# Kernel tuning notes

Measured on AMD Instinct MI355X. Metric: run time of the kernel, lower is better.

The kernel has to match this reference:

```python
import jax, jax.numpy as jnp
import numpy as np
import math

C = 256
GROUPS = 8
EPS = 1e-5


def setup_inputs() -> dict:
    key = jax.random.key(0)
    ks = jax.random.split(key, 12)
    b, c, h, w = 4, C, 64, 64
    s = 1.0 / math.sqrt(c)
    return {
        "x": jax.random.normal(ks[0], (b, c, h, w), dtype=jnp.float32),
        "gamma": jax.random.normal(ks[1], (c,), dtype=jnp.float32) * 0.1 + 1.0,
        "beta": jax.random.normal(ks[2], (c,), dtype=jnp.float32) * 0.1,
        "wq": jax.random.normal(ks[3], (c, c), dtype=jnp.float32) * s,
        "bq": jnp.zeros((c,), dtype=jnp.float32),
        "wk": jax.random.normal(ks[4], (c, c), dtype=jnp.float32) * s,
        "bk": jnp.zeros((c,), dtype=jnp.float32),
        "wv": jax.random.normal(ks[5], (c, c), dtype=jnp.float32) * s,
        "bv": jnp.zeros((c,), dtype=jnp.float32),
        "wp": jax.random.normal(ks[6], (c, c), dtype=jnp.float32) * s,
        "bp": jnp.zeros((c,), dtype=jnp.float32),
    }


def _group_norm(x, gamma, beta):
    b, c, h, w = x.shape
    xg = x.reshape(b, GROUPS, c // GROUPS, h * w)
    mean = xg.mean(axis=(2, 3), keepdims=True)
    var = xg.var(axis=(2, 3), keepdims=True)
    xn = ((xg - mean) * jax.lax.rsqrt(var + EPS)).reshape(b, c, h, w)
    return xn * gamma[None, :, None, None] + beta[None, :, None, None]


def _conv1x1(x, w, b):
    # 1x1 conv == per-pixel channel GEMM
    return jnp.einsum('oc,bchw->bohw', w, x) + b[None, :, None, None]


def reference(x, gamma, beta, wq, bq, wk, bk, wv, bv, wp, bp):
    b, c, h, w = x.shape
    n = h * w
    xn = _group_norm(x, gamma, beta)
    q = _conv1x1(xn, wq, bq).reshape(b, c, n)  # [b,c,n]
    k = _conv1x1(xn, wk, bk).reshape(b, c, n)
    v = _conv1x1(xn, wv, bv).reshape(b, c, n)
    scale = 1.0 / math.sqrt(c)
    scores = jnp.einsum('bcn,bcm->bnm', q, k) * scale  # [b,n,n]
    attn = jax.nn.softmax(scores, axis=-1)
    out = jnp.einsum('bnm,bcm->bcn', attn, v).reshape(b, c, h, w)
    return _conv1x1(out, wp, bp) + x
```

## Files before the change

### kernel.cpp

```cpp
#include <hip/hip_runtime.h>
#include <hip/hip_bf16.h>
#include <math.h>


#define CCH 256
#define NPIX 4096
#define NB 4
#define NG 8
#define EPS 1e-5f
#define NCHUNK 4

typedef __attribute__((ext_vector_type(8))) short short8;
typedef __attribute__((ext_vector_type(4))) short short4v;
typedef __attribute__((ext_vector_type(4))) float f32x4;
typedef unsigned short ushort_t;

#define GLD16(g, l) __builtin_amdgcn_global_load_lds( \
    (const __attribute__((address_space(1))) unsigned int*)(g), \
    (__attribute__((address_space(3))) unsigned int*)(l), 16, 0, 0)

__device__ inline ushort_t f2bf(float x) {
    union { float f; unsigned u; } c; c.f = x;
    unsigned r = c.u + 0x7FFFu + ((c.u >> 16) & 1u);
    return (ushort_t)(r >> 16);
}
__device__ inline float bf2f(ushort_t h) {
    union { unsigned u; float f; } c; c.u = ((unsigned)h) << 16;
    return c.f;
}

__global__ __launch_bounds__(256) void gn1w(const float* __restrict__ x,
                                            const float* __restrict__ wq,
                                            const float* __restrict__ wk,
                                            const float* __restrict__ wv,
                                            const float* __restrict__ wp,
                                            float* __restrict__ part,
                                            ushort_t* __restrict__ wbf,
                                            ushort_t* __restrict__ wpbf) {
    int bid = blockIdx.x;
    int t = threadIdx.x;
    if (bid >= 256) {
        int widx = bid - 256;
        int wi = widx >> 6;
        const float* src = wi == 0 ? wq : wi == 1 ? wk : wi == 2 ? wv : wp;
        ushort_t* dst = wi == 3 ? wpbf : wbf + wi * 65536;
        int i = (widx & 63) * 1024 + t * 4;
        float4 v = *(const float4*)(src + i);
        short4v o;
        o[0] = (short)f2bf(v.x); o[1] = (short)f2bf(v.y);
        o[2] = (short)f2bf(v.z); o[3] = (short)f2bf(v.w);
        *(short4v*)(dst + i) = o;
        return;
    }
    int bg = bid >> 3;
    int slice = bid & 7;
    const float* base = x + (size_t)bg * 32 * NPIX + (size_t)slice * 16384;
    float s = 0.f, sq = 0.f;
    for (int i = t; i < 4096; i += 256) {
        float4 v = ((const float4*)base)[i];
        s  += v.x + v.y + v.z + v.w;
        sq += v.x*v.x + v.y*v.y + v.z*v.z + v.w*v.w;
    }
    for (int off = 32; off; off >>= 1) {
        s  += __shfl_down(s,  off);
        sq += __shfl_down(sq, off);
    }
    __shared__ float red[8];
    int wid = t >> 6;
    if ((t & 63) == 0) { red[wid*2] = s; red[wid*2+1] = sq; }
    __syncthreads();
    if (t == 0) {
        float ts = 0.f, tq = 0.f;
        for (int wv2 = 0; wv2 < 4; wv2++) { ts += red[wv2*2]; tq += red[wv2*2+1]; }
        part[bid*2] = ts; part[bid*2+1] = tq;
    }
}

__global__ __launch_bounds__(256) void gn_transpose(const float* __restrict__ x,
                                                    const float* __restrict__ part,
                                                    const float* __restrict__ gamma,
                                                    const float* __restrict__ beta,
                                                    ushort_t* __restrict__ xnT) {
    __shared__ float T[64][68];
    __shared__ float gmean[2], grstd[2];
    int t = threadIdx.x;
    int nBase = blockIdx.x * 64;
    int cBase = blockIdx.y * 64;
    int b = blockIdx.z;
    if (t < 2) {
        int g = (cBase >> 5) + t;
        float s = 0.f, sq = 0.f;
        for (int i = 0; i < 8; i++) {
            s  += part[((b*NG + g)*8 + i)*2];
            sq += part[((b*NG + g)*8 + i)*2 + 1];
        }
        const float inv = 1.f / 131072.f;
        float mean = s * inv;
        float var = sq * inv - mean * mean;
        gmean[t] = mean;
        grstd[t] = rsqrtf(var + EPS);
    }
    __syncthreads();
    const float* xb = x + (size_t)b * CCH * NPIX;
    int n4  = (t & 15) * 4;
    int cc0 = (t >> 4) * 4;
    for (int i = 0; i < 4; i++) {
        int cc = cc0 + i;
        int c = cBase + cc;
        int gi = cc >> 5;
        float ga = gamma[c] * grstd[gi];
        float be = beta[c] - gmean[gi] * ga;
        float4 v = *(const float4*)&xb[(size_t)c * NPIX + nBase + n4];
        T[cc][n4+0] = v.x * ga + be;
        T[cc][n4+1] = v.y * ga + be;
        T[cc][n4+2] = v.z * ga + be;
        T[cc][n4+3] = v.w * ga + be;
    }
    __syncthreads();
    int nn  = t >> 2;
    int ci0 = (t & 3) * 16;
    short8 o0, o1;
    for (int j = 0; j < 8; j++) {
        o0[j] = (short)f2bf(T[ci0 + j][nn]);
        o1[j] = (short)f2bf(T[ci0 + 8 + j][nn]);
    }
    ushort_t* dst = xnT + ((size_t)b * NPIX + nBase + nn) * CCH + cBase + ci0;
    *(short8*)dst = o0;
    *((short8*)dst + 1) = o1;
}

__global__ __launch_bounds__(256, 2) void qkv3(const ushort_t* __restrict__ xnT,
                                               const ushort_t* __restrict__ wbf,
                                               const float* __restrict__ bq,
                                               const float* __restrict__ bk,
                                               const float* __restrict__ bv,
                                               ushort_t* __restrict__ qT,
                                               ushort_t* __restrict__ kT,
                                               ushort_t* __restrict__ vv) {
    __shared__ __align__(16) ushort_t As[2][4096];
    __shared__ __align__(16) ushort_t Bs[2][4096];
    int t = threadIdx.x;
    int w = t >> 6, l = t & 63, quad = l >> 4, l16 = l & 15;
    int z = blockIdx.z;
    const ushort_t* A; const ushort_t* B; int mBase, nBase;
    if (z < 2) { A = xnT; B = wbf + z * 65536; mBase = blockIdx.x * 128; nBase = blockIdx.y * 128; }
    else       { A = wbf + 131072; B = xnT;    mBase = blockIdx.y * 128; nBase = blockIdx.x * 128; }
    int m0 = (w & 1) * 64, n0 = (w >> 1) * 64;

    const f32x4 fz = {0.f, 0.f, 0.f, 0.f};
    f32x4 acc[4][4];
    #pragma unroll
    for (int i = 0; i < 4; i++)
        #pragma unroll
        for (int j = 0; j < 4; j++) acc[i][j] = fz;

    int srow = t >> 2;
    int slc  = (t & 3) ^ ((t >> 2) & 3);
    int sldso = (t >> 6) * 512;

    #pragma unroll
    for (int j = 0; j < 2; j++) {
        int row = 64*j + srow;
        GLD16(A + (size_t)(mBase + row) * 256 + slc * 8, &As[0][j*2048 + sldso]);
        GLD16(B + (size_t)(nBase + row) * 256 + slc * 8, &Bs[0][j*2048 + sldso]);
    }
    int buf = 0;
    for (int kb = 0; kb < 8; kb++) {
        __syncthreads();
        if (kb < 7) {
            #pragma unroll
            for (int j = 0; j < 2; j++) {
                int row = 64*j + srow;
                GLD16(A + (size_t)(mBase + row) * 256 + (kb+1)*32 + slc * 8, &As[buf^1][j*2048 + sldso]);
                GLD16(B + (size_t)(nBase + row) * 256 + (kb+1)*32 + slc * 8, &Bs[buf^1][j*2048 + sldso]);
            }
        }
        short8 af[4], bfr[4];
        #pragma unroll
        for (int mb = 0; mb < 4; mb++)
            af[mb] = *(short8*)&As[buf][(m0 + mb*16 + l16)*32 + ((quad ^ (l16 & 3)) * 8)];
        #pragma unroll
        for (int nb = 0; nb < 4; nb++)
            bfr[nb] = *(short8*)&Bs[buf][(n0 + nb*16 + l16)*32 + ((quad ^ (l16 & 3)) * 8)];
        #pragma unroll
        for (int mb = 0; mb < 4; mb++)
            #pragma unroll
            for (int nb = 0; nb < 4; nb++)
                acc[mb][nb] = __builtin_amdgcn_mfma_f32_16x16x32_bf16(af[mb], bfr[nb], acc[mb][nb], 0, 0, 0);
        buf ^= 1;
    }
    if (z < 2) {
        const float* bias = z ? bk : bq;
        ushort_t* C = z ? kT : qT;
        #pragma unroll
        for (int nb = 0; nb < 4; nb++) {
            int n = nBase + n0 + nb*16 + l16;
            float bb = bias[n];
            #pragma unroll
            for (int mb = 0; mb < 4; mb++)
                #pragma unroll
                for (int r = 0; r < 4; r++) {
                    int m = mBase + m0 + mb*16 + quad*4 + r;
                    C[(size_t)m * 256 + n] = f2bf(acc[mb][nb][r] + bb);
                }
        }
    } else {
        #pragma unroll
        for (int mb = 0; mb < 4; mb++)
            #pragma unroll
            for (int r = 0; r < 4; r++) {
                int m = mBase + m0 + mb*16 + quad*4 + r;
                float bb = bv[m];
                #pragma unroll
                for (int nb = 0; nb < 4; nb++) {
                    int n = nBase + n0 + nb*16 + l16;
                    vv[((size_t)(n >> 12) * 256 + m) * 4096 + (n & 4095)] = f2bf(acc[mb][nb][r] + bb);
                }
            }
    }
}

__global__ __launch_bounds__(256, 2) void flash_attn(const ushort_t* __restrict__ qT,
                                                     const ushort_t* __restrict__ kT,
                                                     const ushort_t* __restrict__ vv,
                                                     ushort_t* __restrict__ Op0,
                                                     ushort_t* __restrict__ Op1,
                                                     ushort_t* __restrict__ Op2,
                                                     ushort_t* __restrict__ Op3,
                                                     float* __restrict__ lsum) {
    __shared__ __align__(16) ushort_t Ks[2][8192];
    __shared__ __align__(16) ushort_t Vs[2][8192];
    int t = threadIdx.x;
    int w = t >> 6, l = t & 63, quad = l >> 4, l16 = l & 15;
    int qBase = blockIdx.x * 128, chunk = blockIdx.y, b = blockIdx.z;
    int qw = qBase + w * 32;

    short8 qf[2][8];
    #pragma unroll
    for (int s = 0; s < 2; s++) {
        const ushort_t* qrow = qT + ((size_t)b * NPIX + qw + s*16 + l16) * CCH + quad * 8;
        #pragma unroll
        for (int cb = 0; cb < 8; cb++) qf[s][cb] = *(const short8*)(qrow + cb * 32);
    }

    const f32x4 fz = {0.f, 0.f, 0.f, 0.f};
    f32x4 accO[2][16];
    #pragma unroll
    for (int s = 0; s < 2; s++)
        #pragma unroll
        for (int i = 0; i < 16; i++) accO[s][i] = fz;
    float lq[2] = {0.f, 0.f};

    int kr  = t >> 5;
    int klc = (t & 31) ^ kr;
    int vc  = t >> 2;
    int vlc = (t & 3) ^ (vc & 3);
    int sldso = (t >> 6) * 512;
    const ushort_t* kbase = kT + (size_t)b * NPIX * CCH;
    const ushort_t* vbase = vv + (size_t)b * CCH * NPIX;

    const float SC = 0.0625f * 1.44269504089f;
    int mStart = chunk * (NPIX / NCHUNK);
    int mEnd = mStart + NPIX / NCHUNK;

    #pragma unroll
    for (int j = 0; j < 4; j++) {
        GLD16(kbase + (size_t)(mStart + 8*j + kr) * CCH + klc * 8, &Ks[0][j*2048 + sldso]);
        GLD16(vbase + (size_t)(64*j + vc) * NPIX + mStart + vlc * 8, &Vs[0][j*2048 + sldso]);
    }
    int buf = 0;
    for (int mBase = mStart; mBase < mEnd; mBase += 32) {
        __syncthreads();
        if (mBase + 32 < mEnd) {
            #pragma unroll
            for (int j = 0; j < 4; j++) {
                GLD16(kbase + (size_t)(mBase + 32 + 8*j + kr) * CCH + klc * 8, &Ks[buf^1][j*2048 + sldso]);
                GLD16(vbase + (size_t)(64*j + vc) * NPIX + mBase + 32 + vlc * 8, &Vs[buf^1][j*2048 + sldso]);
            }
        }
        f32x4 sT[2][2];
        sT[0][0] = fz; sT[0][1] = fz; sT[1][0] = fz; sT[1][1] = fz;
        #pragma unroll
        for (int cb = 0; cb < 8; cb++) {
            int ksw = ((cb*4 + quad) ^ (l16 & 7)) * 8;
            short8 k0 = *(short8*)&Ks[buf][l16 * 256 + ksw];
            short8 k1 = *(short8*)&Ks[buf][(16 + l16) * 256 + ksw];
            sT[0][0] = __builtin_amdgcn_mfma_f32_16x16x32_bf16(k0, qf[0][cb], sT[0][0], 0, 0, 0);
            sT[1][0] = __builtin_amdgcn_mfma_f32_16x16x32_bf16(k0, qf[1][cb], sT[1][0], 0, 0, 0);
            sT[0][1] = __builtin_amdgcn_mfma_f32_16x16x32_bf16(k1, qf[0][cb], sT[0][1], 0, 0, 0);
            sT[1][1] = __builtin_amdgcn_mfma_f32_16x16x32_bf16(k1, qf[1][cb], sT[1][1], 0, 0, 0);
        }
        short8 pf[2];
        int srcA = ((quad & 1) * 2) * 16 + l16;
        #pragma unroll
        for (int s = 0; s < 2; s++) {
            float ph[2][4];
            #pragma unroll
            for (int h = 0; h < 2; h++)
                #pragma unroll
                for (int r = 0; r < 4; r++) {
                    ph[h][r] = exp2f(sT[s][h][r] * SC);
                    lq[s] += ph[h][r];
                }
            bool hi2 = quad >= 2;
            #pragma unroll
            for (int jj = 0; jj < 4; jj++) {
                float a0 = __shfl(ph[0][jj], srcA);
                float a1 = __shfl(ph[1][jj], srcA);
                float b0 = __shfl(ph[0][jj], srcA + 16);
                float b1 = __shfl(ph[1][jj], srcA + 16);
                pf[s][jj]     = (short)f2bf(hi2 ? a1 : a0);
                pf[s][4 + jj] = (short)f2bf(hi2 ? b1 : b0);
            }
        }
        #pragma unroll
        for (int cblk = 0; cblk < 16; cblk++) {
            short8 vf = *(short8*)&Vs[buf][(cblk*16 + l16)*32 + ((quad ^ (l16 & 3)) * 8)];
            accO[0][cblk] = __builtin_amdgcn_mfma_f32_16x16x32_bf16(vf, pf[0], accO[0][cblk], 0, 0, 0);
            accO[1][cblk] = __builtin_amdgcn_mfma_f32_16x16x32_bf16(vf, pf[1], accO[1][cblk], 0, 0, 0);
        }
        buf ^= 1;
    }

    #pragma unroll
    for (int s = 0; s < 2; s++) {
        float v = lq[s];
        v += __shfl_xor(v, 16);
        v += __shfl_xor(v, 32);
        if (quad == 0)
            lsum[((size_t)chunk * NB + b) * NPIX + qw + s*16 + l16] = v;
    }
    ushort_t* op = chunk == 0 ? Op0 : chunk == 1 ? Op1 : chunk == 2 ? Op2 : Op3;
    #pragma unroll
    for (int s = 0; s < 2; s++) {
        size_t rowb = ((size_t)b * NPIX + qw + s*16 + l16) * CCH;
        #pragma unroll
        for (int cblk = 0; cblk < 16; cblk++) {
            short4v o;
            #pragma unroll
            for (int r = 0; r < 4; r++) o[r] = (short)f2bf(accO[s][cblk][r]);
            *(short4v*)&op[rowb + cblk*16 + quad*4] = o;
        }
    }
}

__global__ __launch_bounds__(256) void attn_combine(ushort_t* __restrict__ Op0,
                                                    const ushort_t* __restrict__ Op1,
                                                    const ushort_t* __restrict__ Op2,
                                                    const ushort_t* __restrict__ Op3,
                                                    const float* __restrict__ lsum) {
    const size_t BN = (size_t)NB * NPIX;
    size_t base = ((size_t)blockIdx.x * 256 + threadIdx.x) * 4;
    size_t bn = base >> 8;
    float li = 1.f / (lsum[bn] + lsum[BN + bn] + lsum[2*BN + bn] + lsum[3*BN + bn]);
    short4v a0 = *(short4v*)&Op0[base];
    short4v a1 = *(const short4v*)&Op1[base];
    short4v a2 = *(const short4v*)&Op2[base];
    short4v a3 = *(const short4v*)&Op3[base];
    short4v o;
    #pragma unroll
    for (int i = 0; i < 4; i++) {
        float v = (bf2f((ushort_t)a0[i]) + bf2f((ushort_t)a1[i]) +
                   bf2f((ushort_t)a2[i]) + bf2f((ushort_t)a3[i])) * li;
        o[i] = (short)f2bf(v);
    }
    *(short4v*)&Op0[base] = o;
}

__global__ __launch_bounds__(256, 2) void projk(const ushort_t* __restrict__ wpbf,
                                                const ushort_t* __restrict__ aoT,
                                                const float* __restrict__ bp,
                                                const float* __restrict__ x,
                                                float* __restrict__ out) {
    __shared__ __align__(16) ushort_t As[2][4096];
    __shared__ __align__(16) ushort_t Bs[2][4096];
    int t = threadIdx.x;
    int w = t >> 6, l = t & 63, quad = l >> 4, l16 = l & 15;
    int mBase = blockIdx.y * 128, nBase = blockIdx.x * 128;
    int m0 = (w & 1) * 64, n0 = (w >> 1) * 64;

    const f32x4 fz = {0.f, 0.f, 0.f, 0.f};
    f32x4 acc[4][4];
    #pragma unroll
    for (int i = 0; i < 4; i++)
        #pragma unroll
        for (int j = 0; j < 4; j++) acc[i][j] = fz;

    int srow = t >> 2;
    int slc  = (t & 3) ^ ((t >> 2) & 3);
    int sldso = (t >> 6) * 512;

    #pragma unroll
    for (int j = 0; j < 2; j++) {
        int row = 64*j + srow;
        GLD16(wpbf + (size_t)(mBase + row) * 256 + slc * 8, &As[0][j*2048 + sldso]);
        GLD16(aoT  + (size_t)(nBase + row) * 256 + slc * 8, &Bs[0][j*2048 + sldso]);
    }
    int buf = 0;
    for (int kb = 0; kb < 8; kb++) {
        __syncthreads();
        if (kb < 7) {
            #pragma unroll
            for (int j = 0; j < 2; j++) {
                int row = 64*j + srow;
                GLD16(wpbf + (size_t)(mBase + row) * 256 + (kb+1)*32 + slc * 8, &As[buf^1][j*2048 + sldso]);
                GLD16(aoT  + (size_t)(nBase + row) * 256 + (kb+1)*32 + slc * 8, &Bs[buf^1][j*2048 + sldso]);
            }
        }
        short8 af[4], bfr[4];
        #pragma unroll
        for (int mb = 0; mb < 4; mb++)
            af[mb] = *(short8*)&As[buf][(m0 + mb*16 + l16)*32 + ((quad ^ (l16 & 3)) * 8)];
        #pragma unroll
        for (int nb = 0; nb < 4; nb++)
            bfr[nb] = *(short8*)&Bs[buf][(n0 + nb*16 + l16)*32 + ((quad ^ (l16 & 3)) * 8)];
        #pragma unroll
        for (int mb = 0; mb < 4; mb++)
            #pragma unroll
            for (int nb = 0; nb < 4; nb++)
                acc[mb][nb] = __builtin_amdgcn_mfma_f32_16x16x32_bf16(af[mb], bfr[nb], acc[mb][nb], 0, 0, 0);
        buf ^= 1;
    }
    #pragma unroll
    for (int mb = 0; mb < 4; mb++)
        #pragma unroll
        for (int r = 0; r < 4; r++) {
            int m = mBase + m0 + mb*16 + quad*4 + r;
            float bb = bp[m];
            #pragma unroll
            for (int nb = 0; nb < 4; nb++) {
                int n = nBase + n0 + nb*16 + l16;
                size_t idx = ((size_t)(n >> 12) * 256 + m) * 4096 + (n & 4095);
                out[idx] = acc[mb][nb][r] + bb + x[idx];
            }
        }
}

extern "C" void kernel_launch(void* const* d_in, const int* in_sizes, int n_in,
                              void* d_out, int out_size, void* d_ws, size_t ws_size,
                              hipStream_t stream) {
    const float* x     = (const float*)d_in[0];
    const float* gamma = (const float*)d_in[1];
    const float* beta  = (const float*)d_in[2];
    const float* wq    = (const float*)d_in[3];
    const float* bq    = (const float*)d_in[4];
    const float* wk    = (const float*)d_in[5];
    const float* bk    = (const float*)d_in[6];
    const float* wv    = (const float*)d_in[7];
    const float* bv    = (const float*)d_in[8];
    const float* wp    = (const float*)d_in[9];
    const float* bp    = (const float*)d_in[10];
    float* out = (float*)d_out;

    const size_t SZ = (size_t)NB * NPIX * CCH;
    float* part  = (float*)d_ws;
    float* lsum  = part + 512;
    ushort_t* wpbf = (ushort_t*)(lsum + (size_t)NCHUNK * NB * NPIX);
    ushort_t* slot0 = wpbf + 65536;
    ushort_t* Op3 = slot0;
    ushort_t* qT  = slot0 + SZ;
    ushort_t* kT  = slot0 + 2*SZ;
    ushort_t* vvp = slot0 + 3*SZ;
    ushort_t* aoT = slot0 + 4*SZ;
    ushort_t* xnT = (ushort_t*)d_out;
    ushort_t* Op1 = (ushort_t*)d_out;
    ushort_t* Op2 = (ushort_t*)d_out + SZ;
    ushort_t* wbf = (ushort_t*)d_out + SZ;

    gn1w<<<512, 256, 0, stream>>>(x, wq, wk, wv, wp, part, wbf, wpbf);
    gn_transpose<<<dim3(64, 4, 4), 256, 0, stream>>>(x, part, gamma, beta, xnT);
    qkv3<<<dim3(128, 2, 3), 256, 0, stream>>>(xnT, wbf, bq, bk, bv, qT, kT, vvp);
    flash_attn<<<dim3(32, NCHUNK, 4), 256, 0, stream>>>(qT, kT, vvp, aoT, Op1, Op2, Op3, lsum);
    attn_combine<<<(int)(SZ / 1024), 256, 0, stream>>>(aoT, Op1, Op2, Op3, lsum);
    projk<<<dim3(128, 2), 256, 0, stream>>>(wpbf, aoT, bp, x, out);
}
```

Before: 228.4 us.

## Switch flash attention MFMAs from 16x16x32 to 32x32x16 tiles

Rewrites the flash attention inner loop to use 32x32x16 bf16 MFMA instructions in place of 16x16x32. Each wave now handles a 32-query tile as a single MFMA output block. The K and V shared-memory swizzles and load mappings are changed to match, and the P fragment is rebuilt with one cross-half shuffle of packed bf16 pairs instead of many per-element shuffles. The goals are fewer LDS fragment reads per FLOP, fewer MFMA issues and less shuffle overhead, at the cost of a new fragment layout that must match the swizzle exactly.

Measured after the change: 250.8 us. 1.1x slower.

```diff
diff --git a/kernel.cpp b/kernel.cpp
--- a/kernel.cpp
+++ b/kernel.cpp
@@ -13,6 +13,7 @@
 typedef __attribute__((ext_vector_type(8))) short short8;
 typedef __attribute__((ext_vector_type(4))) short short4v;
 typedef __attribute__((ext_vector_type(4))) float f32x4;
+typedef __attribute__((ext_vector_type(16))) float f32x16;
 typedef unsigned short ushort_t;
 
 #define GLD16(g, l) __builtin_amdgcn_global_load_lds( \
@@ -231,33 +232,36 @@
     __shared__ __align__(16) ushort_t Ks[2][8192];
     __shared__ __align__(16) ushort_t Vs[2][8192];
     int t = threadIdx.x;
-    int w = t >> 6, l = t & 63, quad = l >> 4, l16 = l & 15;
+    int w = t >> 6, l = t & 63;
+    int l32 = l & 31, hl = l >> 5;
     int qBase = blockIdx.x * 128, chunk = blockIdx.y, b = blockIdx.z;
     int qw = qBase + w * 32;
 
-    short8 qf[2][8];
-    #pragma unroll
-    for (int s = 0; s < 2; s++) {
-        const ushort_t* qrow = qT + ((size_t)b * NPIX + qw + s*16 + l16) * CCH + quad * 8;
-        #pragma unroll
-        for (int cb = 0; cb < 8; cb++) qf[s][cb] = *(const short8*)(qrow + cb * 32);
-    }
-
-    const f32x4 fz = {0.f, 0.f, 0.f, 0.f};
-    f32x4 accO[2][16];
-    #pragma unroll
-    for (int s = 0; s < 2; s++)
-        #pragma unroll
-        for (int i = 0; i < 16; i++) accO[s][i] = fz;
-    float lq[2] = {0.f, 0.f};
-
-    int kr  = t >> 5;
-    int klc = (t & 31) ^ kr;
-    int vc  = t >> 2;
-    int vlc = (t & 3) ^ (vc & 3);
-    int sldso = (t >> 6) * 512;
+    short8 qf[16];
+    {
+        const ushort_t* qrow = qT + ((size_t)b * NPIX + qw + l32) * CCH + hl * 8;
+        #pragma unroll
+        for (int cb = 0; cb < 16; cb++) qf[cb] = *(const short8*)(qrow + cb * 16);
+    }
+
+    f32x16 accO[8];
+    #pragma unroll
+    for (int i = 0; i < 8; i++)
+        #pragma unroll
+        for (int r = 0; r < 16; r++) accO[i][r] = 0.f;
+    float lqa = 0.f;
+
     const ushort_t* kbase = kT + (size_t)b * NPIX * CCH;
     const ushort_t* vbase = vv + (size_t)b * CCH * NPIX;
+    int sldso = w * 512;
+
+    int kkv[4], kko[4], vcc[4], vvo[4];
+    #pragma unroll
+    for (int j = 0; j < 4; j++) {
+        int n = j*256 + t;
+        kkv[j] = n >> 5; kko[j] = (n & 31) ^ (kkv[j] & 7);
+        vcc[j] = n >> 2; vvo[j] = (n & 3) ^ ((vcc[j] >> 1) & 3);
+    }
 
     const float SC = 0.0625f * 1.44269504089f;
     int mStart = chunk * (NPIX / NCHUNK);
@@ -265,8 +269,8 @@
 
     #pragma unroll
     for (int j = 0; j < 4; j++) {
-        GLD16(kbase + (size_t)(mStart + 8*j + kr) * CCH + klc * 8, &Ks[0][j*2048 + sldso]);
-        GLD16(vbase + (size_t)(64*j + vc) * NPIX + mStart + vlc * 8, &Vs[0][j*2048 + sldso]);
+        GLD16(kbase + (size_t)(mStart + kkv[j]) * CCH + kko[j] * 8, &Ks[0][j*2048 + sldso]);
+        GLD16(vbase + (size_t)vcc[j] * NPIX + mStart + vvo[j] * 8, &Vs[0][j*2048 + sldso]);
     }
     int buf = 0;
     for (int mBase = mStart; mBase < mEnd; mBase += 32) {
@@ -274,74 +278,72 @@
         if (mBase + 32 < mEnd) {
             #pragma unroll
             for (int j = 0; j < 4; j++) {
-                GLD16(kbase + (size_t)(mBase + 32 + 8*j + kr) * CCH + klc * 8, &Ks[buf^1][j*2048 + sldso]);
-                GLD16(vbase + (size_t)(64*j + vc) * NPIX + mBase + 32 + vlc * 8, &Vs[buf^1][j*2048 + sldso]);
+                GLD16(kbase + (size_t)(mBase + 32 + kkv[j]) * CCH + kko[j] * 8, &Ks[buf^1][j*2048 + sldso]);
+                GLD16(vbase + (size_t)vcc[j] * NPIX + mBase + 32 + vvo[j] * 8, &Vs[buf^1][j*2048 + sldso]);
             }
         }
-        f32x4 sT[2][2];
-        sT[0][0] = fz; sT[0][1] = fz; sT[1][0] = fz; sT[1][1] = fz;
-        #pragma unroll
-        for (int cb = 0; cb < 8; cb++) {
-            int ksw = ((cb*4 + quad) ^ (l16 & 7)) * 8;
-            short8 k0 = *(short8*)&Ks[buf][l16 * 256 + ksw];
-            short8 k1 = *(short8*)&Ks[buf][(16 + l16) * 256 + ksw];
-            sT[0][0] = __builtin_amdgcn_mfma_f32_16x16x32_bf16(k0, qf[0][cb], sT[0][0], 0, 0, 0);
-            sT[1][0] = __builtin_amdgcn_mfma_f32_16x16x32_bf16(k0, qf[1][cb], sT[1][0], 0, 0, 0);
-            sT[0][1] = __builtin_amdgcn_mfma_f32_16x16x32_bf16(k1, qf[0][cb], sT[0][1], 0, 0, 0);
-            sT[1][1] = __builtin_amdgcn_mfma_f32_16x16x32_bf16(k1, qf[1][cb], sT[1][1], 0, 0, 0);
-        }
-        short8 pf[2];
-        int srcA = ((quad & 1) * 2) * 16 + l16;
-        #pragma unroll
-        for (int s = 0; s < 2; s++) {
-            float ph[2][4];
-            #pragma unroll
-            for (int h = 0; h < 2; h++)
-                #pragma unroll
-                for (int r = 0; r < 4; r++) {
-                    ph[h][r] = exp2f(sT[s][h][r] * SC);
-                    lq[s] += ph[h][r];
-                }
-            bool hi2 = quad >= 2;
-            #pragma unroll
-            for (int jj = 0; jj < 4; jj++) {
-                float a0 = __shfl(ph[0][jj], srcA);
-                float a1 = __shfl(ph[1][jj], srcA);
-                float b0 = __shfl(ph[0][jj], srcA + 16);
-                float b1 = __shfl(ph[1][jj], srcA + 16);
-                pf[s][jj]     = (short)f2bf(hi2 ? a1 : a0);
-                pf[s][4 + jj] = (short)f2bf(hi2 ? b1 : b0);
-            }
-        }
-        #pragma unroll
-        for (int cblk = 0; cblk < 16; cblk++) {
-            short8 vf = *(short8*)&Vs[buf][(cblk*16 + l16)*32 + ((quad ^ (l16 & 3)) * 8)];
-            accO[0][cblk] = __builtin_amdgcn_mfma_f32_16x16x32_bf16(vf, pf[0], accO[0][cblk], 0, 0, 0);
-            accO[1][cblk] = __builtin_amdgcn_mfma_f32_16x16x32_bf16(vf, pf[1], accO[1][cblk], 0, 0, 0);
+        f32x16 sT;
+        #pragma unroll
+        for (int r = 0; r < 16; r++) sT[r] = 0.f;
+        #pragma unroll
+        for (int cb = 0; cb < 16; cb++) {
+            int ko = (cb*2 + hl) ^ (l32 & 7);
+            short8 kf = *(short8*)&Ks[buf][l32*256 + ko*8];
+            sT = __builtin_amdgcn_mfma_f32_32x32x16_bf16(kf, qf[cb], sT, 0, 0, 0);
+        }
+        unsigned pk[8], sw[8];
+        float part = 0.f;
+        #pragma unroll
+        for (int i = 0; i < 8; i++) {
+            float p0 = exp2f(sT[2*i]   * SC);
+            float p1 = exp2f(sT[2*i+1] * SC);
+            part += p0 + p1;
+            pk[i] = ((unsigned)f2bf(p1) << 16) | (unsigned)f2bf(p0);
+        }
+        lqa += part;
+        #pragma unroll
+        for (int i = 0; i < 8; i++) sw[i] = (unsigned)__shfl_xor((int)pk[i], 32);
+        unsigned f1u[4], f2u[4];
+        if (hl == 0) {
+            f1u[0]=pk[0]; f1u[1]=pk[1]; f1u[2]=sw[0]; f1u[3]=sw[1];
+            f2u[0]=pk[4]; f2u[1]=pk[5]; f2u[2]=sw[4]; f2u[3]=sw[5];
+        } else {
+            f1u[0]=sw[2]; f1u[1]=sw[3]; f1u[2]=pk[2]; f1u[3]=pk[3];
+            f2u[0]=sw[6]; f2u[1]=sw[7]; f2u[2]=pk[6]; f2u[3]=pk[7];
+        }
+        short8 pf1, pf2;
+        #pragma unroll
+        for (int i = 0; i < 4; i++) {
+            ((unsigned*)&pf1)[i] = f1u[i];
+            ((unsigned*)&pf2)[i] = f2u[i];
+        }
+        #pragma unroll
+        for (int cblk = 0; cblk < 8; cblk++) {
+            int c = cblk*32 + l32;
+            short8 vf1 = *(short8*)&Vs[buf][(c*4 + ((0*2+hl) ^ ((c>>1)&3)))*8];
+            short8 vf2 = *(short8*)&Vs[buf][(c*4 + ((1*2+hl) ^ ((c>>1)&3)))*8];
+            accO[cblk] = __builtin_amdgcn_mfma_f32_32x32x16_bf16(vf1, pf1, accO[cblk], 0, 0, 0);
+            accO[cblk] = __builtin_amdgcn_mfma_f32_32x32x16_bf16(vf2, pf2, accO[cblk], 0, 0, 0);
         }
         buf ^= 1;
     }
 
-    #pragma unroll
-    for (int s = 0; s < 2; s++) {
-        float v = lq[s];
-        v += __shfl_xor(v, 16);
-        v += __shfl_xor(v, 32);
-        if (quad == 0)
-            lsum[((size_t)chunk * NB + b) * NPIX + qw + s*16 + l16] = v;
+    {
+        float v = lqa + __shfl_xor(lqa, 32);
+        if (hl == 0)
+            lsum[((size_t)chunk * NB + b) * NPIX + qw + l32] = v;
     }
     ushort_t* op = chunk == 0 ? Op0 : chunk == 1 ? Op1 : chunk == 2 ? Op2 : Op3;
-    #pragma unroll
-    for (int s = 0; s < 2; s++) {
-        size_t rowb = ((size_t)b * NPIX + qw + s*16 + l16) * CCH;
-        #pragma unroll
-        for (int cblk = 0; cblk < 16; cblk++) {
+    size_t rowb = ((size_t)b * NPIX + qw + l32) * CCH;
+    #pragma unroll
+    for (int cblk = 0; cblk < 8; cblk++)
+        #pragma unroll
+        for (int a = 0; a < 4; a++) {
             short4v o;
             #pragma unroll
-            for (int r = 0; r < 4; r++) o[r] = (short)f2bf(accO[s][cblk][r]);
-            *(short4v*)&op[rowb + cblk*16 + quad*4] = o;
-        }
-    }
+            for (int r = 0; r < 4; r++) o[r] = (short)f2bf(accO[cblk][a*4 + r]);
+            *(short4v*)&op[rowb + cblk*32 + a*8 + hl*4] = o;
+        }
 }
 
 __global__ __launch_bounds__(256) void attn_combine(ushort_t* __restrict__ Op0,
```
